# Kernel tuning notes

Hardware: AMD Instinct MI355X
Metric: run time of the kernel (lower is better)

## Reference

```python
import jax, jax.numpy as jnp
import numpy as np

EMBED_DIM = 1024
NUM_HEADS = 16
HEAD_DIM = EMBED_DIM // NUM_HEADS


def setup_inputs() -> dict:
    key = jax.random.key(0)
    k_x, k_qkv, k_ow, k_ob = jax.random.split(key, 4)
    B, N, D = 4, 2048, EMBED_DIM
    x = jax.random.normal(k_x, (B, N, D), dtype=jnp.float32)
    # nn.Linear(D, 3D, bias=False): weight [3D, D], y = x @ W.T
    w_qkv = jax.random.normal(k_qkv, (3 * D, D), dtype=jnp.float32) * (D ** -0.5)
    # nn.Linear(D, D): weight [D, D], bias [D]
    w_out = jax.random.normal(k_ow, (D, D), dtype=jnp.float32) * (D ** -0.5)
    b_out = jax.random.normal(k_ob, (D,), dtype=jnp.float32) * 0.01
    return {"x": x, "w_qkv": w_qkv, "w_out": w_out, "b_out": b_out}


def reference(x, w_qkv, w_out, b_out):
    B, N, D = x.shape
    H, Hd = NUM_HEADS, HEAD_DIM
    scale = Hd ** -0.5
    qkv = x @ w_qkv.T                              # [B, N, 3D]
    q, k, v = jnp.split(qkv, 3, axis=-1)
    q = q.reshape(B, N, H, Hd).transpose(0, 2, 1, 3)  # [B, H, N, Hd]
    k = k.reshape(B, N, H, Hd).transpose(0, 2, 1, 3)
    v = v.reshape(B, N, H, Hd).transpose(0, 2, 1, 3)
    scores = jnp.einsum('bhnd,bhmd->bhnm', q, k) * scale  # [B, H, N, N]
    attn = jax.nn.softmax(scores, axis=-1)
    out = jnp.einsum('bhnm,bhmd->bhnd', attn, v)   # [B, H, N, Hd]
    out = out.transpose(0, 2, 1, 3).reshape(B, N, D)
    return out @ w_out.T + b_out
```

## Files before the change

kernel.cpp:

```cpp
#include <hip/hip_runtime.h>
#include <math.h>

#define SEQ   2048
#define BATCH 4
#define NH    16
#define HD    64
#define DDIM  1024

typedef __attribute__((ext_vector_type(8))) short short8;
typedef __attribute__((ext_vector_type(4))) float f32x4;

#define QSCALE 0.18033688011112042f
#define C2     14.426950408889634f

#if __has_builtin(__builtin_amdgcn_exp2f)
#define EXP2(x) __builtin_amdgcn_exp2f(x)
#else
#define EXP2(x) exp2f(x)
#endif

__device__ __forceinline__ ushort f2bf(float f) {
  union { float f; unsigned u; } x; x.f = f;
  unsigned r = x.u + 0x7fffu + ((x.u >> 16) & 1u);
  return (ushort)(r >> 16);
}

#if __has_builtin(__builtin_amdgcn_cvt_pk_bf16_f32)
typedef __attribute__((ext_vector_type(2))) __bf16 bf16x2;
__device__ __forceinline__ unsigned pk2bf(float a, float b) {
  union { bf16x2 v; unsigned u; } x;
  x.v = __builtin_amdgcn_cvt_pk_bf16_f32(a, b);
  return x.u;
}
#else
__device__ __forceinline__ unsigned pk2bf(float a, float b) {
  return (unsigned)f2bf(a) | ((unsigned)f2bf(b) << 16);
}
#endif

__device__ __forceinline__ void gll16(const ushort* g, ushort* l) {
  __builtin_amdgcn_global_load_lds(
      (const __attribute__((address_space(1))) unsigned int*)g,
      (__attribute__((address_space(3))) unsigned int*)l, 16, 0, 0);
}

__global__ __launch_bounds__(256) void conv_bf16(
    const float* __restrict__ in, ushort* __restrict__ out) {
  size_t i = ((size_t)blockIdx.x * 256 + threadIdx.x) * 4;
  float4 v = *(const float4*)(in + i);
  uint2 u;
  u.x = pk2bf(v.x, v.y);
  u.y = pk2bf(v.z, v.w);
  *(uint2*)(out + i) = u;
}

__device__ __forceinline__ void gemm_nt_core(
    const ushort* __restrict__ A, const ushort* __restrict__ B,
    ushort* As, ushort* Bs, f32x4 (&acc)[4][4], int m0, int n0) {
  const int tid = threadIdx.x;
  const int lane = tid & 63;
  const int w = tid >> 6;
  const int KD = 1024;

  const int rA = lane >> 2;
  const int gg = (lane & 3) ^ ((lane >> 3) & 3);
  const ushort* ag0 = A + (size_t)(m0 + w * 32 + rA) * KD + gg * 8;
  const ushort* ag1 = ag0 + (size_t)16 * KD;
  const ushort* bg0 = B + (size_t)(n0 + w * 32 + rA) * KD + gg * 8;
  const ushort* bg1 = bg0 + (size_t)16 * KD;
  ushort* al0 = As + (w * 32) * 32;  ushort* al1 = al0 + 16 * 32;
  ushort* bl0 = Bs + (w * 32) * 32;  ushort* bl1 = bl0 + 16 * 32;

  const int fr = lane & 15;
  const int fg = lane >> 4;
  const int fo = (fg ^ ((fr >> 1) & 3)) * 8;
  const int wm = (w & 1) * 64, wn = (w >> 1) * 64;

  for (int kt = 0; kt < KD; kt += 32) {
    __syncthreads();
    gll16(ag0 + kt, al0);
    gll16(ag1 + kt, al1);
    gll16(bg0 + kt, bl0);
    gll16(bg1 + kt, bl1);
    __syncthreads();
    short8 af[4], bf[4];
#pragma unroll
    for (int t = 0; t < 4; ++t) {
      af[t] = *(const short8*)&As[(wm + t * 16 + fr) * 32 + fo];
      bf[t] = *(const short8*)&Bs[(wn + t * 16 + fr) * 32 + fo];
    }
#pragma unroll
    for (int mt = 0; mt < 4; ++mt)
#pragma unroll
      for (int nt = 0; nt < 4; ++nt)
        acc[mt][nt] = __builtin_amdgcn_mfma_f32_16x16x32_bf16(
            af[mt], bf[nt], acc[mt][nt], 0, 0, 0);
  }
}

__global__ __launch_bounds__(256) void gemm_qkv(
    const ushort* __restrict__ A, const ushort* __restrict__ B,
    ushort* __restrict__ Qb, ushort* __restrict__ Kb, ushort* __restrict__ Vtb) {
  __shared__ ushort smem[9216];
  ushort* As = smem;
  ushort* Bs = smem + 4096;
  const int m0 = blockIdx.y * 128, n0 = blockIdx.x * 128;
  f32x4 acc[4][4] = {};
  gemm_nt_core(A, B, As, Bs, acc, m0, n0);

  const int lane = threadIdx.x & 63;
  const int w = threadIdx.x >> 6;
  const int wm = (w & 1) * 64, wn = (w >> 1) * 64;
  const int cr = (lane >> 4) * 4;
  const int cc = lane & 15;

  if (n0 >= 2048) {
    ushort* T = smem;
    const int b = m0 >> 11;
    const int rbase = m0 & 2047;
    const int tid = threadIdx.x;
#pragma unroll
    for (int p = 0; p < 2; ++p) {
      __syncthreads();
      if ((w >> 1) == p) {
#pragma unroll
        for (int mt = 0; mt < 4; ++mt)
#pragma unroll
          for (int nt = 0; nt < 4; ++nt) {
            const int nl = nt * 16 + cc;
            const int ml = wm + mt * 16 + cr;
#pragma unroll
            for (int jp = 0; jp < 2; ++jp) {
              unsigned u = pk2bf(acc[mt][nt][2 * jp], acc[mt][nt][2 * jp + 1]);
              *(unsigned*)&T[nl * 138 + ml + 2 * jp] = u;
            }
          }
      }
      __syncthreads();
      const int nl = tid >> 2, c0 = (tid & 3) * 32;
      const int d = (n0 - 2048) + p * 64 + nl;
      const int h = d >> 6, dd = d & 63;
      ushort* gdst = Vtb + ((size_t)(b * 16 + h) * 64 + dd) * 2048 + rbase + c0;
#pragma unroll
      for (int q = 0; q < 4; ++q)
        *(short8*)(gdst + q * 8) = *(const short8*)&T[nl * 138 + c0 + q * 8];
    }
  } else {
    const float qs = (n0 < 1024) ? QSCALE : 1.0f;
    ushort* dst = (n0 < 1024) ? Qb : Kb;
    const int nb = (n0 < 1024) ? n0 : n0 - 1024;
#pragma unroll
    for (int mt = 0; mt < 4; ++mt) {
#pragma unroll
      for (int nt = 0; nt < 4; ++nt) {
        const int n = nb + wn + nt * 16 + cc;
        const int h = n >> 6, d = n & 63;
#pragma unroll
        for (int j = 0; j < 4; ++j) {
          const int m = m0 + wm + mt * 16 + cr + j;
          const int b = m >> 11, r = m & 2047;
          dst[(((size_t)(b * 16 + h) * 2048 + r) << 6) + d] =
              f2bf(acc[mt][nt][j] * qs);
        }
      }
    }
  }
}

__global__ __launch_bounds__(256) void gemm_out(
    const ushort* __restrict__ A, const ushort* __restrict__ B,
    const float* __restrict__ bias, float* __restrict__ C) {
  __shared__ ushort smem[8192];
  ushort* As = smem;
  ushort* Bs = smem + 4096;
  const int m0 = blockIdx.y * 128, n0 = blockIdx.x * 128;
  f32x4 acc[4][4] = {};
  gemm_nt_core(A, B, As, Bs, acc, m0, n0);

  const int lane = threadIdx.x & 63;
  const int w = threadIdx.x >> 6;
  const int wm = (w & 1) * 64, wn = (w >> 1) * 64;
  const int cr = (lane >> 4) * 4;
  const int cc = lane & 15;
#pragma unroll
  for (int mt = 0; mt < 4; ++mt) {
#pragma unroll
    for (int nt = 0; nt < 4; ++nt) {
      const int n = n0 + wn + nt * 16 + cc;
      const float bj = bias[n];
#pragma unroll
      for (int j = 0; j < 4; ++j) {
        const int m = m0 + wm + mt * 16 + cr + j;
        C[(size_t)m * 1024 + n] = acc[mt][nt][j] + bj;
      }
    }
  }
}

__global__ __launch_bounds__(256, 3) void attn_bf16(
    const ushort* __restrict__ Qb, const ushort* __restrict__ Kb,
    const ushort* __restrict__ Vtb, ushort* __restrict__ attn) {
  const int b = blockIdx.z, h = blockIdx.y, q0 = blockIdx.x * 128;
  const int tid = threadIdx.x, lane = tid & 63, w = tid >> 6;

  __shared__ ushort Qs[128 * 64];
  __shared__ ushort Ks[2][64 * 64];
  __shared__ ushort Vts[2][64 * 64];

  const size_t head = (size_t)(b * 16 + h) * (2048 * 64);

#pragma unroll
  for (int pass = 0; pass < 2; ++pass) {
    const int r = pass * 64 + (tid >> 2), cb = (tid & 3) * 2;
    const ushort* qp = Qb + head + (size_t)(q0 + r) * 64 + cb * 8;
    short8 a = *(const short8*)qp;
    short8 bv = *(const short8*)(qp + 8);
    const int sw = r & 7;
    *(short8*)&Qs[r * 64 + ((cb ^ sw) * 8)] = a;
    *(short8*)&Qs[r * 64 + (((cb + 1) ^ sw) * 8)] = bv;
  }

  const int rk = lane >> 3;
  const int c7 = lane & 7;
  const ushort* kg0 = Kb + head + (size_t)(w * 16 + rk) * 64 + ((c7 ^ (rk & 3)) * 8);
  const ushort* kg1 = Kb + head + (size_t)(w * 16 + 8 + rk) * 64 + ((c7 ^ (rk & 3) ^ 4) * 8);
  const ushort* vg0 = Vtb + head + (size_t)(w * 16 + rk) * 2048 + (c7 ^ rk) * 8;
  const ushort* vg1 = vg0 + 8 * 2048;
  ushort* klb[2] = {&Ks[0][(w * 16) * 64], &Ks[1][(w * 16) * 64]};
  ushort* vlb[2] = {&Vts[0][(w * 16) * 64], &Vts[1][(w * 16) * 64]};

  const int fr = lane & 15;
  const int fg = lane >> 4;
  const int fr7 = fr & 7;
  const int rbK = ((fr >> 2) * 8 + (fr & 3)) * 64;
  const int slK = (fr & 3) | (((fr >> 2) & 1) << 2);

  const short8 ones = {0x3F80, 0x3F80, 0x3F80, 0x3F80,
                       0x3F80, 0x3F80, 0x3F80, 0x3F80};

  f32x4 oacc[2][4] = {};
  f32x4 racc[2] = {};

  gll16(kg0, klb[0]);
  gll16(kg1, klb[0] + 8 * 64);
  gll16(vg0, vlb[0]);
  gll16(vg1, vlb[0] + 8 * 64);

  for (int kt = 0; kt < SEQ / 64; ++kt) {
    __syncthreads();
    const int cur = kt & 1;
    if (kt + 1 < SEQ / 64) {
      const int nxt = cur ^ 1;
      gll16(kg0 + (kt + 1) * 4096, klb[nxt]);
      gll16(kg1 + (kt + 1) * 4096, klb[nxt] + 8 * 64);
      gll16(vg0 + (kt + 1) * 64, vlb[nxt]);
      gll16(vg1 + (kt + 1) * 64, vlb[nxt] + 8 * 64);
    }
    const ushort* K = &Ks[cur][0];
    const ushort* V = &Vts[cur][0];

    f32x4 sacc[2][4];
#pragma unroll
    for (int qs = 0; qs < 2; ++qs)
#pragma unroll
      for (int l = 0; l < 4; ++l)
        sacc[qs][l] = (f32x4){-C2, -C2, -C2, -C2};
#pragma unroll
    for (int kd = 0; kd < 2; ++kd) {
      const int qo = ((kd * 4 + fg) ^ fr7) * 8;
      short8 aq0 = *(const short8*)&Qs[(w * 32 + fr) * 64 + qo];
      short8 aq1 = *(const short8*)&Qs[(w * 32 + 16 + fr) * 64 + qo];
      const int ko = ((kd * 4 + fg) ^ slK) * 8;
#pragma unroll
      for (int l = 0; l < 4; ++l) {
        short8 bk = *(const short8*)&K[(l >> 1) * 2048 + (l & 1) * 256 + rbK + ko];
        sacc[0][l] = __builtin_amdgcn_mfma_f32_16x16x32_bf16(bk, aq0, sacc[0][l], 0, 0, 0);
        sacc[1][l] = __builtin_amdgcn_mfma_f32_16x16x32_bf16(bk, aq1, sacc[1][l], 0, 0, 0);
      }
    }

    short8 pa[2][2];
#pragma unroll
    for (int qs = 0; qs < 2; ++qs) {
#pragma unroll
      for (int kg = 0; kg < 2; ++kg) {
        const float e0 = EXP2(sacc[qs][2 * kg][0]);
        const float e1 = EXP2(sacc[qs][2 * kg][1]);
        const float e2 = EXP2(sacc[qs][2 * kg][2]);
        const float e3 = EXP2(sacc[qs][2 * kg][3]);
        const float e4 = EXP2(sacc[qs][2 * kg + 1][0]);
        const float e5 = EXP2(sacc[qs][2 * kg + 1][1]);
        const float e6 = EXP2(sacc[qs][2 * kg + 1][2]);
        const float e7 = EXP2(sacc[qs][2 * kg + 1][3]);
        union { unsigned u[4]; short8 s8; } P;
        P.u[0] = pk2bf(e0, e1);
        P.u[1] = pk2bf(e2, e3);
        P.u[2] = pk2bf(e4, e5);
        P.u[3] = pk2bf(e6, e7);
        pa[qs][kg] = P.s8;
      }
    }

#pragma unroll
    for (int kg = 0; kg < 2; ++kg) {
      const int vo = ((kg * 4 + fg) ^ fr7) * 8;
#pragma unroll
      for (int nt = 0; nt < 4; ++nt) {
        short8 bv = *(const short8*)&V[(nt * 16 + fr) * 64 + vo];
        oacc[0][nt] = __builtin_amdgcn_mfma_f32_16x16x32_bf16(pa[0][kg], bv, oacc[0][nt], 0, 0, 0);
        oacc[1][nt] = __builtin_amdgcn_mfma_f32_16x16x32_bf16(pa[1][kg], bv, oacc[1][nt], 0, 0, 0);
      }
      racc[0] = __builtin_amdgcn_mfma_f32_16x16x32_bf16(pa[0][kg], ones, racc[0], 0, 0, 0);
      racc[1] = __builtin_amdgcn_mfma_f32_16x16x32_bf16(pa[1][kg], ones, racc[1], 0, 0, 0);
    }
  }

#pragma unroll
  for (int qs = 0; qs < 2; ++qs) {
#pragma unroll
    for (int j = 0; j < 4; ++j) {
      const float invj = 1.f / racc[qs][j];
      const int row = q0 + w * 32 + qs * 16 + fg * 4 + j;
#pragma unroll
      for (int nt = 0; nt < 4; ++nt) {
        attn[(size_t)(b * SEQ + row) * DDIM + h * 64 + nt * 16 + fr] =
            f2bf(oacc[qs][nt][j] * invj);
      }
    }
  }
}

extern "C" void kernel_launch(void* const* d_in, const int* in_sizes, int n_in,
                              void* d_out, int out_size, void* d_ws, size_t ws_size,
                              hipStream_t stream) {
  const float* x     = (const float*)d_in[0];
  const float* w_qkv = (const float*)d_in[1];
  const float* w_out = (const float*)d_in[2];
  const float* b_out = (const float*)d_in[3];
  float* out = (float*)d_out;

  ushort* Ax    = (ushort*)d_ws;
  ushort* Wq    = Ax + (size_t)8192 * 1024;
  ushort* Wo    = Wq + (size_t)3072 * 1024;
  ushort* Qb    = Wo + (size_t)1024 * 1024;
  ushort* Kb    = Qb + (size_t)BATCH * NH * SEQ * HD;
  ushort* Vtb   = Kb + (size_t)BATCH * NH * SEQ * HD;
  ushort* attnb = Vtb + (size_t)BATCH * NH * SEQ * HD;

  conv_bf16<<<8192, 256, 0, stream>>>(x, Ax);
  conv_bf16<<<3072, 256, 0, stream>>>(w_qkv, Wq);
  conv_bf16<<<1024, 256, 0, stream>>>(w_out, Wo);

  gemm_qkv<<<dim3(3072 / 128, 8192 / 128), 256, 0, stream>>>(Ax, Wq, Qb, Kb, Vtb);
  attn_bf16<<<dim3(SEQ / 128, NH, BATCH), 256, 0, stream>>>(Qb, Kb, Vtb, attnb);
  gemm_out<<<dim3(1024 / 128, 8192 / 128), 256, 0, stream>>>(attnb, Wo, b_out, out);
}
```

Before: 277.6 us.

## Merge bf16 conversion launches and unroll attention K/V loop by two

The three fp32-to-bf16 conversion kernels become one launch that selects its source by block index, writing into the contiguous workspace (Ax, Wq and Wo are laid out back to back). The attention inner loop is manually unrolled by two with static double-buffer pointers, so the LDS buffer indexing and the per-iteration prefetch branch go away. The first QK MFMA now takes the -C2 init constant directly as its accumulator instead of copying it in first. These changes target launch overhead and loop bookkeeping, at the cost of more code inside the attention kernel and possibly higher register pressure.

```diff
diff --git a/kernel.cpp b/kernel.cpp
--- a/kernel.cpp
+++ b/kernel.cpp
@@ -44,14 +44,20 @@
       (__attribute__((address_space(3))) unsigned int*)l, 16, 0, 0);
 }
 
-__global__ __launch_bounds__(256) void conv_bf16(
-    const float* __restrict__ in, ushort* __restrict__ out) {
-  size_t i = ((size_t)blockIdx.x * 256 + threadIdx.x) * 4;
-  float4 v = *(const float4*)(in + i);
+__global__ __launch_bounds__(256) void conv_bf16_all(
+    const float* __restrict__ x, const float* __restrict__ wq,
+    const float* __restrict__ wo, ushort* __restrict__ dst) {
+  const int gid = blockIdx.x;
+  const float* src;
+  if (gid < 8192)       src = x  + (size_t)gid * 1024;
+  else if (gid < 11264) src = wq + (size_t)(gid - 8192) * 1024;
+  else                  src = wo + (size_t)(gid - 11264) * 1024;
+  const size_t i = (size_t)threadIdx.x * 4;
+  float4 v = *(const float4*)(src + i);
   uint2 u;
   u.x = pk2bf(v.x, v.y);
   u.y = pk2bf(v.z, v.w);
-  *(uint2*)(out + i) = u;
+  *(uint2*)(dst + (size_t)gid * 1024 + i) = u;
 }
 
 __device__ __forceinline__ void gemm_nt_core(
@@ -226,8 +232,8 @@
   const ushort* kg1 = Kb + head + (size_t)(w * 16 + 8 + rk) * 64 + ((c7 ^ (rk & 3) ^ 4) * 8);
   const ushort* vg0 = Vtb + head + (size_t)(w * 16 + rk) * 2048 + (c7 ^ rk) * 8;
   const ushort* vg1 = vg0 + 8 * 2048;
-  ushort* klb[2] = {&Ks[0][(w * 16) * 64], &Ks[1][(w * 16) * 64]};
-  ushort* vlb[2] = {&Vts[0][(w * 16) * 64], &Vts[1][(w * 16) * 64]};
+  ushort* kl0 = &Ks[0][(w * 16) * 64];  ushort* kl1 = &Ks[1][(w * 16) * 64];
+  ushort* vl0 = &Vts[0][(w * 16) * 64]; ushort* vl1 = &Vts[1][(w * 16) * 64];
 
   const int fr = lane & 15;
   const int fg = lane >> 4;
@@ -237,40 +243,30 @@
 
   const short8 ones = {0x3F80, 0x3F80, 0x3F80, 0x3F80,
                        0x3F80, 0x3F80, 0x3F80, 0x3F80};
+  const f32x4 cinit = {-C2, -C2, -C2, -C2};
 
   f32x4 oacc[2][4] = {};
   f32x4 racc[2] = {};
 
-  gll16(kg0, klb[0]);
-  gll16(kg1, klb[0] + 8 * 64);
-  gll16(vg0, vlb[0]);
-  gll16(vg1, vlb[0] + 8 * 64);
-
-  for (int kt = 0; kt < SEQ / 64; ++kt) {
-    __syncthreads();
-    const int cur = kt & 1;
-    if (kt + 1 < SEQ / 64) {
-      const int nxt = cur ^ 1;
-      gll16(kg0 + (kt + 1) * 4096, klb[nxt]);
-      gll16(kg1 + (kt + 1) * 4096, klb[nxt] + 8 * 64);
-      gll16(vg0 + (kt + 1) * 64, vlb[nxt]);
-      gll16(vg1 + (kt + 1) * 64, vlb[nxt] + 8 * 64);
-    }
-    const ushort* K = &Ks[cur][0];
-    const ushort* V = &Vts[cur][0];
-
+  auto tile_step = [&](const ushort* K, const ushort* V) {
     f32x4 sacc[2][4];
-#pragma unroll
-    for (int qs = 0; qs < 2; ++qs)
-#pragma unroll
-      for (int l = 0; l < 4; ++l)
-        sacc[qs][l] = (f32x4){-C2, -C2, -C2, -C2};
-#pragma unroll
-    for (int kd = 0; kd < 2; ++kd) {
-      const int qo = ((kd * 4 + fg) ^ fr7) * 8;
+    {
+      const int qo = (fg ^ fr7) * 8;
       short8 aq0 = *(const short8*)&Qs[(w * 32 + fr) * 64 + qo];
       short8 aq1 = *(const short8*)&Qs[(w * 32 + 16 + fr) * 64 + qo];
-      const int ko = ((kd * 4 + fg) ^ slK) * 8;
+      const int ko = (fg ^ slK) * 8;
+#pragma unroll
+      for (int l = 0; l < 4; ++l) {
+        short8 bk = *(const short8*)&K[(l >> 1) * 2048 + (l & 1) * 256 + rbK + ko];
+        sacc[0][l] = __builtin_amdgcn_mfma_f32_16x16x32_bf16(bk, aq0, cinit, 0, 0, 0);
+        sacc[1][l] = __builtin_amdgcn_mfma_f32_16x16x32_bf16(bk, aq1, cinit, 0, 0, 0);
+      }
+    }
+    {
+      const int qo = ((4 + fg) ^ fr7) * 8;
+      short8 aq0 = *(const short8*)&Qs[(w * 32 + fr) * 64 + qo];
+      short8 aq1 = *(const short8*)&Qs[(w * 32 + 16 + fr) * 64 + qo];
+      const int ko = ((4 + fg) ^ slK) * 8;
 #pragma unroll
       for (int l = 0; l < 4; ++l) {
         short8 bk = *(const short8*)&K[(l >> 1) * 2048 + (l & 1) * 256 + rbK + ko];
@@ -313,6 +309,30 @@
       racc[0] = __builtin_amdgcn_mfma_f32_16x16x32_bf16(pa[0][kg], ones, racc[0], 0, 0, 0);
       racc[1] = __builtin_amdgcn_mfma_f32_16x16x32_bf16(pa[1][kg], ones, racc[1], 0, 0, 0);
     }
+  };
+
+  gll16(kg0, kl0);
+  gll16(kg1, kl0 + 8 * 64);
+  gll16(vg0, vl0);
+  gll16(vg1, vl0 + 8 * 64);
+
+#pragma unroll 1
+  for (int kt = 0; kt < SEQ / 64; kt += 2) {
+    __syncthreads();
+    gll16(kg0 + (kt + 1) * 4096, kl1);
+    gll16(kg1 + (kt + 1) * 4096, kl1 + 8 * 64);
+    gll16(vg0 + (kt + 1) * 64, vl1);
+    gll16(vg1 + (kt + 1) * 64, vl1 + 8 * 64);
+    tile_step(&Ks[0][0], &Vts[0][0]);
+
+    __syncthreads();
+    if (kt + 2 < SEQ / 64) {
+      gll16(kg0 + (kt + 2) * 4096, kl0);
+      gll16(kg1 + (kt + 2) * 4096, kl0 + 8 * 64);
+      gll16(vg0 + (kt + 2) * 64, vl0);
+      gll16(vg1 + (kt + 2) * 64, vl0 + 8 * 64);
+    }
+    tile_step(&Ks[1][0], &Vts[1][0]);
   }
 
 #pragma unroll
@@ -347,9 +367,7 @@
   ushort* Vtb   = Kb + (size_t)BATCH * NH * SEQ * HD;
   ushort* attnb = Vtb + (size_t)BATCH * NH * SEQ * HD;
 
-  conv_bf16<<<8192, 256, 0, stream>>>(x, Ax);
-  conv_bf16<<<3072, 256, 0, stream>>>(w_qkv, Wq);
-  conv_bf16<<<1024, 256, 0, stream>>>(w_out, Wo);
+  conv_bf16_all<<<12288, 256, 0, stream>>>(x, w_qkv, w_out, Ax);
 
   gemm_qkv<<<dim3(3072 / 128, 8192 / 128), 256, 0, stream>>>(Ax, Wq, Qb, Kb, Vtb);
   attn_bf16<<<dim3(SEQ / 128, NH, BATCH), 256, 0, stream>>>(Qb, Kb, Vtb, attnb);
```

Result: no change. 279.6 us (+0.7%).
